# Performance work log

Measured on AMD Instinct MI355X. Metric: run time of the kernel, lower is better.

Reference implementation:

```python
import jax, jax.numpy as jnp
import numpy as np
from jax import lax

B, SEQ, CIN = 8, 4096, 7
DM, NL, PL = 512, 4, 16
NP = SEQ // PL            # 256 patches
NS, DC, EXP = 16, 4, 2
DI = EXP * DM             # 1024 inner dim
DTR = (DM + 15) // 16     # 32 dt_rank (mamba_ssm default ceil(d_model/16))
CD, PRED = 64, 96
EPS = 1e-5


def setup_inputs() -> dict:
    key = jax.random.key(0)
    ks = jax.random.split(key, 16)
    r = lambda k, s, sc=0.02: jax.random.normal(k, s, jnp.float32) * sc
    A_row = jnp.arange(1, NS + 1, dtype=jnp.float32)
    return {
        "x": jax.random.normal(ks[0], (B, SEQ, CIN), jnp.float32),
        "in_g": jnp.ones((CIN,), jnp.float32), "in_b": jnp.zeros((CIN,), jnp.float32),
        "pe_W": r(ks[1], (DM, CIN, PL), 0.1), "pe_b": jnp.zeros((DM,), jnp.float32),
        "ln_g": jnp.ones((NL, DM), jnp.float32), "ln_b": jnp.zeros((NL, DM), jnp.float32),
        "W_in": r(ks[2], (NL, 2 * DI, DM)),
        "conv_W": r(ks[3], (NL, DI, 1, DC), 0.2), "conv_b": jnp.zeros((NL, DI), jnp.float32),
        "W_x": r(ks[4], (NL, DTR + 2 * NS, DI)),
        "W_dt": r(ks[5], (NL, DI, DTR), 0.1),
        "b_dt": jnp.full((NL, DI), -4.6, jnp.float32),  # softplus^-1(~0.01)
        "A_log": jnp.log(jnp.tile(A_row, (NL, DI, 1))),
        "Dskip": jnp.ones((NL, DI), jnp.float32),
        "W_out": r(ks[6], (NL, DM, DI)),
        "fn_g": jnp.ones((DM,), jnp.float32), "fn_b": jnp.zeros((DM,), jnp.float32),
        "hW1": r(ks[7], (2 * CD, DM * NP)), "hb1": jnp.zeros((2 * CD,), jnp.float32),
        "hW2": r(ks[8], (PRED, 2 * CD)), "hb2": jnp.zeros((PRED,), jnp.float32),
    }


def layernorm(x, g, b):
    m = jnp.mean(x, axis=-1, keepdims=True)
    v = jnp.mean((x - m) ** 2, axis=-1, keepdims=True)
    return (x - m) * lax.rsqrt(v + EPS) * g + b


def silu(x):
    return x * jax.nn.sigmoid(x)


def selective_scan(dA, dBx, C):
    # dA, dBx: (B, L, DI, N);  C: (B, L, N)  ->  y: (B, L, DI)
    def step(h, t):
        dA_t, dbx_t, c_t = t
        h = dA_t * h + dbx_t                      # (B, DI, N)
        y = jnp.einsum('bdn,bn->bd', h, c_t)
        return h, y
    h0 = jnp.zeros((dA.shape[0], DI, NS), dA.dtype)
    _, ys = lax.scan(step, h0, (dA.transpose(1, 0, 2, 3), dBx.transpose(1, 0, 2, 3), C.transpose(1, 0, 2)))
    return ys.transpose(1, 0, 2)


def mamba_block(u, W_in, cW, cb, W_x, W_dt, b_dt, A_log, Dv, W_out):
    xz = jnp.einsum('bld,ed->ble', u, W_in)       # (B, L, 2*DI)
    xi, z = jnp.split(xz, 2, axis=-1)
    # causal depthwise conv over time
    xc = lax.conv_general_dilated(xi.transpose(0, 2, 1), cW, (1,), [(DC - 1, 0)],
                                  feature_group_count=DI,
                                  dimension_numbers=('NCH', 'OIH', 'NCH'))
    xc = silu(xc + cb[None, :, None]).transpose(0, 2, 1)  # (B, L, DI)
    dbl = jnp.einsum('bld,ed->ble', xc, W_x)      # (B, L, DTR + 2*NS)
    dt, Bm, Cm = dbl[..., :DTR], dbl[..., DTR:DTR + NS], dbl[..., DTR + NS:]
    delta = jax.nn.softplus(jnp.einsum('blr,dr->bld', dt, W_dt) + b_dt)  # (B, L, DI)
    A = -jnp.exp(A_log)                           # (DI, NS)
    dA = jnp.exp(delta[..., None] * A)            # (B, L, DI, NS)
    dBx = delta[..., None] * Bm[:, :, None, :] * xc[..., None]
    y = selective_scan(dA, dBx, Cm)
    y = (y + xc * Dv) * silu(z)
    return jnp.einsum('bld,od->blo', y, W_out)


def reference(x, in_g, in_b, pe_W, pe_b, ln_g, ln_b, W_in, conv_W, conv_b,
              W_x, W_dt, b_dt, A_log, Dskip, W_out, fn_g, fn_b, hW1, hb1, hW2, hb2):
    h = layernorm(x, in_g, in_b)
    # patch embed: stride==kernel Conv1d == per-patch matmul
    p = h.reshape(B, NP, PL, CIN)
    h = jnp.einsum('bnpc,dcp->bnd', p, pe_W) + pe_b   # (B, NP, DM)
    for i in range(NL):
        res = h
        h = layernorm(h, ln_g[i], ln_b[i])
        h = mamba_block(h, W_in[i], conv_W[i], conv_b[i], W_x[i], W_dt[i],
                        b_dt[i], A_log[i], Dskip[i], W_out[i])
        h = h + res                                   # dropout is identity at eval
    h = layernorm(h, fn_g, fn_b)
    h = h.reshape(B, -1)                              # (B, DM*NP)
    h = jax.nn.gelu(h @ hW1.T + hb1, approximate=False)
    return h @ hW2.T + hb2                            # (B, PRED)
```

## Files before the change

kernel.cpp:

```cpp
#include <hip/hip_runtime.h>
#include <hip/hip_bf16.h>
#include <math.h>

#define B_    8
#define SEQ_  4096
#define CIN_  7
#define DM_   512
#define NL_   4
#define PL_   16
#define NP_   256
#define NS_   16
#define DC_   4
#define DI_   1024
#define DTR_  32
#define CD_   64
#define PRED_ 96
#define TOK_  (B_*NP_)
#define EPS_  1e-5f
#define CL_   16
#define NCH_  (NP_/CL_)

typedef unsigned short u16;
typedef __attribute__((ext_vector_type(8))) short short8;
typedef __attribute__((ext_vector_type(4))) float floatx4;

__device__ __forceinline__ float silu_f(float x){ return x / (1.f + __expf(-x)); }
__device__ __forceinline__ float softplus_f(float x){ return x > 20.f ? x : log1pf(__expf(x)); }
__device__ __forceinline__ u16 f2bf(float f){
  union { __hip_bfloat16 h; u16 u; } cv; cv.h = __float2bfloat16(f); return cv.u;
}
#define GLDS16(g, l) __builtin_amdgcn_global_load_lds( \
    (const __attribute__((address_space(1))) void*)(g), \
    (__attribute__((address_space(3))) void*)(l), 16, 0, 0)

__global__ void ln7_kernel(const float* __restrict__ x, const float* __restrict__ g,
                           const float* __restrict__ b, u16* __restrict__ xpb){
  int i = blockIdx.x*256 + threadIdx.x;
  if (i >= B_*SEQ_) return;
  float v[CIN_]; float m = 0.f;
  #pragma unroll
  for (int c=0;c<CIN_;c++){ v[c]=x[i*CIN_+c]; m+=v[c]; }
  m *= (1.f/CIN_);
  float var = 0.f;
  #pragma unroll
  for (int c=0;c<CIN_;c++){ float d=v[c]-m; var+=d*d; }
  var *= (1.f/CIN_);
  float r = rsqrtf(var + EPS_);
  int bn = i >> 4, p = i & 15;
  u16* row = xpb + (size_t)bn*128;
  #pragma unroll
  for (int c=0;c<CIN_;c++) row[c*16+p] = f2bf((v[c]-m)*r*g[c]+b[c]);
  row[112+p] = 0;
}

__global__ __launch_bounds__(256) void ln512_kernel(const float* __restrict__ in,
    const float* __restrict__ g, const float* __restrict__ b,
    float* __restrict__ out, u16* __restrict__ outb){
  int tid = threadIdx.x;
  int wv = tid>>6, lane = tid&63;
  int t = blockIdx.x*4 + wv;
  const float4* row = (const float4*)(in + (size_t)t*DM_);
  float4 v0 = row[lane], v1 = row[64+lane];
  float s = v0.x+v0.y+v0.z+v0.w + v1.x+v1.y+v1.z+v1.w;
  #pragma unroll
  for (int o=1;o<64;o<<=1) s += __shfl_xor(s,o);
  float m = s*(1.f/DM_);
  float d0x=v0.x-m,d0y=v0.y-m,d0z=v0.z-m,d0w=v0.w-m;
  float d1x=v1.x-m,d1y=v1.y-m,d1z=v1.z-m,d1w=v1.w-m;
  float q = d0x*d0x+d0y*d0y+d0z*d0z+d0w*d0w + d1x*d1x+d1y*d1y+d1z*d1z+d1w*d1w;
  #pragma unroll
  for (int o=1;o<64;o<<=1) q += __shfl_xor(q,o);
  float r = rsqrtf(q*(1.f/DM_) + EPS_);
  float4 g0 = ((const float4*)g)[lane], g1 = ((const float4*)g)[64+lane];
  float4 b0 = ((const float4*)b)[lane], b1 = ((const float4*)b)[64+lane];
  float4 o0 = { d0x*r*g0.x+b0.x, d0y*r*g0.y+b0.y, d0z*r*g0.z+b0.z, d0w*r*g0.w+b0.w };
  float4 o1 = { d1x*r*g1.x+b1.x, d1y*r*g1.y+b1.y, d1z*r*g1.z+b1.z, d1w*r*g1.w+b1.w };
  ((float4*)(out + (size_t)t*DM_))[lane]    = o0;
  ((float4*)(out + (size_t)t*DM_))[64+lane] = o1;
  ushort4 p0 = { f2bf(o0.x), f2bf(o0.y), f2bf(o0.z), f2bf(o0.w) };
  ushort4 p1 = { f2bf(o1.x), f2bf(o1.y), f2bf(o1.z), f2bf(o1.w) };
  ((ushort4*)(outb + (size_t)t*DM_))[lane]    = p0;
  ((ushort4*)(outb + (size_t)t*DM_))[64+lane] = p1;
}

template<int BM, int BN, bool ACC, bool BIAS>
__global__ __launch_bounds__(256) void gemm_bf16(const u16* __restrict__ A,
    const u16* __restrict__ Bw, float* __restrict__ C, const float* __restrict__ bias,
    int K, int lda, int ldb, int ldc){
  constexpr int MI = BM/32, NI = BN/32;
  __shared__ __align__(16) u16 As[BM*64];
  __shared__ __align__(16) u16 Bs[BN*64];
  int tid = threadIdx.x;
  int wave = __builtin_amdgcn_readfirstlane(tid>>6);
  int lane = tid&63;
  int wm = wave>>1, wn = wave&1;
  int quad = lane>>4, l16 = lane&15;
  int bm = blockIdx.y*BM, bn = blockIdx.x*BN;
  int r8 = lane>>3, sseg = lane&7;
  int gseg = sseg ^ r8;
  floatx4 acc[MI][NI] = {};
  for (int k0 = 0; k0 < K; k0 += 64){
    #pragma unroll
    for (int r = 0; r < BM/32; r++){
      int rowb = (r*4 + wave)*8;
      const u16* gp = A + (size_t)(bm + rowb + r8)*lda + k0 + gseg*8;
      GLDS16(gp, &As[rowb*64]);
    }
    #pragma unroll
    for (int r = 0; r < BN/32; r++){
      int rowb = (r*4 + wave)*8;
      const u16* gp = Bw + (size_t)(bn + rowb + r8)*ldb + k0 + gseg*8;
      GLDS16(gp, &Bs[rowb*64]);
    }
    __syncthreads();
    #pragma unroll
    for (int kh = 0; kh < 2; kh++){
      short8 af[MI], bfr[NI];
      #pragma unroll
      for (int i = 0; i < MI; i++){
        int row = wm*(BM/2)+i*16+l16;
        af[i] = *(short8*)&As[row*64 + (((kh*4+quad)^(row&7))*8)];
      }
      #pragma unroll
      for (int j = 0; j < NI; j++){
        int row = wn*(BN/2)+j*16+l16;
        bfr[j] = *(short8*)&Bs[row*64 + (((kh*4+quad)^(row&7))*8)];
      }
      #pragma unroll
      for (int i = 0; i < MI; i++)
        #pragma unroll
        for (int j = 0; j < NI; j++)
          acc[i][j] = __builtin_amdgcn_mfma_f32_16x16x32_bf16(af[i], bfr[j], acc[i][j], 0, 0, 0);
    }
    __syncthreads();
  }
  #pragma unroll
  for (int i = 0; i < MI; i++){
    #pragma unroll
    for (int j = 0; j < NI; j++){
      #pragma unroll
      for (int r = 0; r < 4; r++){
        int m  = bm + wm*(BM/2) + i*16 + quad*4 + r;
        int nn = bn + wn*(BN/2) + j*16 + l16;
        float v = acc[i][j][r];
        if (ACC) C[(size_t)m*ldc+nn] += v;
        else     C[(size_t)m*ldc+nn]  = BIAS ? v + bias[nn] : v;
      }
    }
  }
}

__global__ __launch_bounds__(256) void dblpart_kernel(const u16* __restrict__ A,
    const u16* __restrict__ Bw, float* __restrict__ part){
  __shared__ __align__(16) u16 As[64*64];
  __shared__ __align__(16) u16 Bs[64*64];
  int tid = threadIdx.x;
  int wave = __builtin_amdgcn_readfirstlane(tid>>6);
  int lane = tid&63;
  int wm = wave>>1, wn = wave&1;
  int quad = lane>>4, l16 = lane&15;
  int bm = blockIdx.x*64;
  int kc = blockIdx.y;
  int r8 = lane>>3, sseg = lane&7;
  int gseg = sseg ^ r8;
  floatx4 acc[2][2] = {};
  for (int k0 = kc*256; k0 < kc*256 + 256; k0 += 64){
    #pragma unroll
    for (int r = 0; r < 2; r++){
      int rowb = (r*4 + wave)*8;
      GLDS16(A  + (size_t)(bm + rowb + r8)*DI_ + k0 + gseg*8, &As[rowb*64]);
      GLDS16(Bw + (size_t)(     rowb + r8)*DI_ + k0 + gseg*8, &Bs[rowb*64]);
    }
    __syncthreads();
    #pragma unroll
    for (int kh = 0; kh < 2; kh++){
      short8 af[2], bfr[2];
      #pragma unroll
      for (int i = 0; i < 2; i++){
        int row = wm*32+i*16+l16;
        af[i] = *(short8*)&As[row*64 + (((kh*4+quad)^(row&7))*8)];
      }
      #pragma unroll
      for (int j = 0; j < 2; j++){
        int row = wn*32+j*16+l16;
        bfr[j] = *(short8*)&Bs[row*64 + (((kh*4+quad)^(row&7))*8)];
      }
      #pragma unroll
      for (int i = 0; i < 2; i++)
        #pragma unroll
        for (int j = 0; j < 2; j++)
          acc[i][j] = __builtin_amdgcn_mfma_f32_16x16x32_bf16(af[i], bfr[j], acc[i][j], 0, 0, 0);
    }
    __syncthreads();
  }
  float* dst = part + (size_t)kc*TOK_*64;
  #pragma unroll
  for (int i = 0; i < 2; i++)
    #pragma unroll
    for (int j = 0; j < 2; j++)
      #pragma unroll
      for (int r = 0; r < 4; r++){
        int m  = bm + wm*32 + i*16 + quad*4 + r;
        int nn = wn*32 + j*16 + l16;
        dst[(size_t)m*64+nn] = acc[i][j][r];
      }
}

__global__ __launch_bounds__(256) void dblsum_kernel(const float* __restrict__ part,
    float* __restrict__ dbl){
  int idx = blockIdx.x*256 + threadIdx.x;
  float4 a = ((const float4*)part)[idx];
  float4 b = ((const float4*)(part + (size_t)TOK_*64))[idx];
  float4 c = ((const float4*)(part + (size_t)2*TOK_*64))[idx];
  float4 d = ((const float4*)(part + (size_t)3*TOK_*64))[idx];
  float4 o = { a.x+b.x+c.x+d.x, a.y+b.y+c.y+d.y, a.z+b.z+c.z+d.z, a.w+b.w+c.w+d.w };
  ((float4*)dbl)[idx] = o;
}

__global__ void conv_silu_kernel(const float* __restrict__ xz, const float* __restrict__ cW,
                                 const float* __restrict__ cb, float* __restrict__ xc,
                                 u16* __restrict__ xcb){
  int idx = blockIdx.x*256 + threadIdx.x;
  if (idx >= TOK_*DI_/4) return;
  int c4 = idx & (DI_/4 - 1); int t = idx >> 8;
  int l = t & (NP_-1);
  int c = c4*4;
  float4 acc = *(const float4*)&cb[c];
  float wa[4], wb[4], wc[4], wd[4];
  *(float4*)wa = *(const float4*)&cW[(c+0)*DC_];
  *(float4*)wb = *(const float4*)&cW[(c+1)*DC_];
  *(float4*)wc = *(const float4*)&cW[(c+2)*DC_];
  *(float4*)wd = *(const float4*)&cW[(c+3)*DC_];
  const float* base = xz + (size_t)t*(2*DI_) + c;
  #pragma unroll
  for (int k = 0; k < DC_; k++){
    if (l - 3 + k >= 0){
      float4 xv = *(const float4*)(base + (k-3)*(2*DI_));
      acc.x += xv.x*wa[k];
      acc.y += xv.y*wb[k];
      acc.z += xv.z*wc[k];
      acc.w += xv.w*wd[k];
    }
  }
  acc.x = silu_f(acc.x); acc.y = silu_f(acc.y);
  acc.z = silu_f(acc.z); acc.w = silu_f(acc.w);
  *(float4*)&xc[(size_t)t*DI_ + c] = acc;
  ushort4 pb = { f2bf(acc.x), f2bf(acc.y), f2bf(acc.z), f2bf(acc.w) };
  *(ushort4*)&xcb[(size_t)t*DI_ + c] = pb;
}

__global__ __launch_bounds__(256) void delta_kernel(const float* __restrict__ dbl,
    const float* __restrict__ wdtT, const float* __restrict__ bdt, float* __restrict__ delta){
  __shared__ float sdt[16][DTR_];
  int tid = threadIdx.x;
  int t0 = blockIdx.y*16;
  int d = blockIdx.x*256 + tid;
  for (int i = tid; i < 16*DTR_; i += 256){
    int t = i >> 5, r = i & 31;
    sdt[t][r] = dbl[(size_t)(t0 + t)*64 + r];
  }
  float wv[DTR_];
  #pragma unroll
  for (int r = 0; r < DTR_; r++) wv[r] = wdtT[(size_t)r*DI_ + d];
  float bb = bdt[d];
  __syncthreads();
  #pragma unroll 4
  for (int t = 0; t < 16; t++){
    float acc = bb;
    #pragma unroll
    for (int r = 0; r < DTR_; r++) acc += sdt[t][r]*wv[r];
    delta[(size_t)(t0 + t)*DI_ + d] = softplus_f(acc);
  }
}

__global__ __launch_bounds__(256) void scan_part_kernel(const float* __restrict__ delta,
    const float* __restrict__ xc, const float* __restrict__ dbl,
    const float* __restrict__ Alog, float* __restrict__ hend, float* __restrict__ aprod){
  __shared__ float sBC[CL_][32];
  int tid = threadIdx.x;
  int d = blockIdx.x*256 + tid;
  int bych = blockIdx.y;
  int b = bych >> 4, ch = bych & (NCH_-1);
  int base = b*NP_ + ch*CL_;
  for (int i = tid; i < CL_*32; i += 256){
    int t = i >> 5, c = i & 31;
    sBC[t][c] = dbl[(size_t)(base+t)*64 + 32 + c];
  }
  float A[NS_], h[NS_], pr[NS_];
  #pragma unroll
  for (int k = 0; k < NS_; k++){
    A[k] = -__expf(Alog[(size_t)d*NS_ + k]);
    h[k] = 0.f; pr[k] = 1.f;
  }
  __syncthreads();
  #pragma unroll
  for (int t = 0; t < CL_; t++){
    int row = base + t;
    float de = delta[(size_t)row*DI_ + d];
    float xv = xc[(size_t)row*DI_ + d];
    float cde = de*xv;
    #pragma unroll
    for (int k = 0; k < NS_; k++){
      float a = __expf(de*A[k]);
      h[k] = a*h[k] + cde*sBC[t][k];
      pr[k] *= a;
    }
  }
  size_t o = ((size_t)bych*DI_ + d)*NS_;
  #pragma unroll
  for (int k = 0; k < NS_; k++){ hend[o+k] = h[k]; aprod[o+k] = pr[k]; }
}

__global__ __launch_bounds__(256) void scan_fix_kernel(const float* __restrict__ aprod,
    float* __restrict__ hend){
  int id = blockIdx.x*256 + threadIdx.x;
  int nd = id & (DI_*NS_ - 1);
  int b  = id >> 14;
  float h = 0.f;
  #pragma unroll
  for (int ch = 0; ch < NCH_; ch++){
    size_t idx = (size_t)(b*NCH_ + ch)*(DI_*NS_) + nd;
    float ap = aprod[idx];
    float he = hend[idx];
    hend[idx] = h;
    h = ap*h + he;
  }
}

__global__ __launch_bounds__(256) void scan_final_kernel(const float* __restrict__ delta,
    const float* __restrict__ xc, const float* __restrict__ dbl,
    const float* __restrict__ xz, const float* __restrict__ Dv,
    const float* __restrict__ Alog, const float* __restrict__ hin,
    u16* __restrict__ yb){
  __shared__ float sBC[CL_][32];
  int tid = threadIdx.x;
  int d = blockIdx.x*256 + tid;
  int bych = blockIdx.y;
  int b = bych >> 4, ch = bych & (NCH_-1);
  int base = b*NP_ + ch*CL_;
  for (int i = tid; i < CL_*32; i += 256){
    int t = i >> 5, c = i & 31;
    sBC[t][c] = dbl[(size_t)(base+t)*64 + 32 + c];
  }
  float A[NS_], h[NS_];
  size_t o = ((size_t)bych*DI_ + d)*NS_;
  #pragma unroll
  for (int k = 0; k < NS_; k++){
    A[k] = -__expf(Alog[(size_t)d*NS_ + k]);
    h[k] = hin[o + k];
  }
  float Dvd = Dv[d];
  __syncthreads();
  #pragma unroll
  for (int t = 0; t < CL_; t++){
    int row = base + t;
    float de = delta[(size_t)row*DI_ + d];
    float xv = xc[(size_t)row*DI_ + d];
    float zz = xz[(size_t)row*(2*DI_) + DI_ + d];
    float cde = de*xv;
    float p = 0.f;
    #pragma unroll
    for (int k = 0; k < NS_; k++){
      float a = __expf(de*A[k]);
      h[k] = a*h[k] + cde*sBC[t][k];
      p += h[k]*sBC[t][16+k];
    }
    yb[(size_t)row*DI_ + d] = f2bf((p + xv*Dvd) * silu_f(zz));
  }
}

__global__ __launch_bounds__(256) void head1_kernel(const float* __restrict__ u,
    const float* __restrict__ hW1, float* __restrict__ partial){
  const int KTOT = DM_*NP_;
  int nb = blockIdx.x;
  int kc = blockIdx.y;
  int tid = threadIdx.x;
  int lane = tid & 63, wv = tid >> 6;
  int n = nb*4 + wv;
  const float* wrow = hW1 + (size_t)n*KTOT;
  float acc[8] = {};
  int kb = kc*1024 + lane*4;
  #pragma unroll
  for (int it = 0; it < 4; it++){
    int k = kb + it*256;
    float4 w4 = *(const float4*)&wrow[k];
    #pragma unroll
    for (int m = 0; m < 8; m++){
      float4 u4 = *(const float4*)&u[(size_t)m*KTOT + k];
      acc[m] += u4.x*w4.x + u4.y*w4.y + u4.z*w4.z + u4.w*w4.w;
    }
  }
  #pragma unroll
  for (int m = 0; m < 8; m++){
    float v = acc[m];
    v += __shfl_xor(v,1); v += __shfl_xor(v,2); v += __shfl_xor(v,4);
    v += __shfl_xor(v,8); v += __shfl_xor(v,16); v += __shfl_xor(v,32);
    acc[m] = v;
  }
  if (lane == 0){
    float* dst = partial + ((size_t)kc*128 + n)*8;
    #pragma unroll
    for (int m = 0; m < 8; m++) dst[m] = acc[m];
  }
}

__global__ void head_combine_kernel(const float* __restrict__ partial,
    const float* __restrict__ hb1, float* __restrict__ t1){
  int idx = blockIdx.x*256 + threadIdx.x;
  if (idx >= 128*8) return;
  int n = idx >> 3, m = idx & 7;
  float s = hb1[n];
  for (int kc = 0; kc < 128; kc++) s += partial[((size_t)kc*128 + n)*8 + m];
  float ge = 0.5f*s*(1.f + erff(s*0.70710678118f));
  t1[m*128 + n] = ge;
}

__global__ void head2_kernel(const float* __restrict__ t1, const float* __restrict__ hW2,
                             const float* __restrict__ hb2, float* __restrict__ out){
  int idx = blockIdx.x*128 + threadIdx.x;
  if (idx >= B_*PRED_) return;
  int m = idx / PRED_, q = idx % PRED_;
  float s = hb2[q];
  #pragma unroll 16
  for (int k = 0; k < 2*CD_; k++) s += t1[m*128 + k]*hW2[q*128 + k];
  out[idx] = s;
}

__global__ __launch_bounds__(256) void prep_kernel(const float* __restrict__ W_dt,
    const float* __restrict__ W_x, const float* __restrict__ W_in,
    const float* __restrict__ W_out, const float* __restrict__ peW,
    float* __restrict__ wdtT, u16* __restrict__ wxB,
    u16* __restrict__ WinB, u16* __restrict__ WoutB, u16* __restrict__ peWb){
  int idx = blockIdx.x*256 + threadIdx.x;
  {
    float4 v = ((const float4*)W_in)[idx];
    ushort4 o = { f2bf(v.x), f2bf(v.y), f2bf(v.z), f2bf(v.w) };
    ((ushort4*)WinB)[idx] = o;
  }
  if (idx < 524288){
    float4 v = ((const float4*)W_out)[idx];
    ushort4 o = { f2bf(v.x), f2bf(v.y), f2bf(v.z), f2bf(v.w) };
    ((ushort4*)WoutB)[idx] = o;
  }
  if (idx < NL_*64*DI_/4){
    float4 v = ((const float4*)W_x)[idx];
    ushort4 o = { f2bf(v.x), f2bf(v.y), f2bf(v.z), f2bf(v.w) };
    ((ushort4*)wxB)[idx] = o;
  }
  if (idx < NL_*DTR_*DI_){
    int l = idx / (DTR_*DI_); int rem = idx % (DTR_*DI_);
    int r = rem / DI_; int d = rem % DI_;
    wdtT[idx] = W_dt[((size_t)l*DI_ + d)*DTR_ + r];
  }
  if (idx < 512*128){
    int d = idx >> 7, kk = idx & 127;
    peWb[idx] = (kk < 112) ? f2bf(peW[d*112 + kk]) : (u16)0;
  }
}

extern "C" void kernel_launch(void* const* d_in, const int* in_sizes, int n_in,
                              void* d_out, int out_size, void* d_ws, size_t ws_size,
                              hipStream_t stream) {
  const float* x      = (const float*)d_in[0];
  const float* in_g   = (const float*)d_in[1];
  const float* in_b   = (const float*)d_in[2];
  const float* pe_W   = (const float*)d_in[3];
  const float* pe_b   = (const float*)d_in[4];
  const float* ln_g   = (const float*)d_in[5];
  const float* ln_b   = (const float*)d_in[6];
  const float* W_in   = (const float*)d_in[7];
  const float* conv_W = (const float*)d_in[8];
  const float* conv_b = (const float*)d_in[9];
  const float* W_x    = (const float*)d_in[10];
  const float* W_dt   = (const float*)d_in[11];
  const float* b_dt   = (const float*)d_in[12];
  const float* A_log  = (const float*)d_in[13];
  const float* Dskip  = (const float*)d_in[14];
  const float* W_out  = (const float*)d_in[15];
  const float* fn_g   = (const float*)d_in[16];
  const float* fn_b   = (const float*)d_in[17];
  const float* hW1    = (const float*)d_in[18];
  const float* hb1    = (const float*)d_in[19];
  const float* hW2    = (const float*)d_in[20];
  const float* hb2    = (const float*)d_in[21];

  float* ws    = (float*)d_ws;
  float* h     = ws;
  float* un    = h     + 1048576;
  float* xz    = un    + 1048576;
  float* xc    = xz    + 4194304;
  float* dblb  = xc    + 2097152;
  float* delta = dblb  + 131072;
  float* y     = delta + 2097152;
  float* wdtT  = y     + 2097152;
  u16*   wxB   = (u16*)(wdtT + 131072);
  float* bf_rgn= wdtT + 131072 + 131072;
  u16*   unb   = (u16*)bf_rgn;
  u16*   yb    = (u16*)(bf_rgn + 524288);
  u16*   WinB  = (u16*)(bf_rgn + 524288 + 1048576);
  u16*   WoutB = (u16*)(bf_rgn + 524288 + 1048576 + 2097152);
  u16*   peWb  = (u16*)(bf_rgn + 524288 + 1048576 + 2097152 + 1048576);
  float* aprod = bf_rgn + 524288 + 1048576 + 2097152 + 1048576 + 32768;
  float* hend  = y;
  u16*   xcb   = (u16*)y;
  u16*   xpb   = (u16*)y;
  float* dblpart = aprod;
  float* partial = xz;
  float* t1      = xz + 262144;

  prep_kernel<<<4096, 256, 0, stream>>>(W_dt, W_x, W_in, W_out, pe_W,
                                        wdtT, wxB, WinB, WoutB, peWb);
  ln7_kernel<<<(B_*SEQ_+255)/256, 256, 0, stream>>>(x, in_g, in_b, xpb);
  gemm_bf16<64,128,false,true><<<dim3(DM_/128, TOK_/64), 256, 0, stream>>>(
      xpb, peWb, h, pe_b, 128, 128, 128, DM_);

  for (int l = 0; l < NL_; l++){
    ln512_kernel<<<TOK_/4, 256, 0, stream>>>(h, ln_g + l*DM_, ln_b + l*DM_, un, unb);
    gemm_bf16<64,128,false,false><<<dim3(2*DI_/128, TOK_/64), 256, 0, stream>>>(
        unb, WinB + (size_t)l*2*DI_*DM_, xz, nullptr, DM_, DM_, DM_, 2*DI_);
    conv_silu_kernel<<<(TOK_*DI_/4)/256, 256, 0, stream>>>(
        xz, conv_W + (size_t)l*DI_*DC_, conv_b + (size_t)l*DI_, xc, xcb);
    dblpart_kernel<<<dim3(TOK_/64, 4), 256, 0, stream>>>(
        xcb, wxB + (size_t)l*64*DI_, dblpart);
    dblsum_kernel<<<(TOK_*64/4)/256, 256, 0, stream>>>(dblpart, dblb);
    delta_kernel<<<dim3(DI_/256, TOK_/16), 256, 0, stream>>>(
        dblb, wdtT + (size_t)l*DTR_*DI_, b_dt + (size_t)l*DI_, delta);
    scan_part_kernel<<<dim3(DI_/256, B_*NCH_), 256, 0, stream>>>(
        delta, xc, dblb, A_log + (size_t)l*DI_*NS_, hend, aprod);
    scan_fix_kernel<<<(B_*DI_*NS_)/256, 256, 0, stream>>>(aprod, hend);
    scan_final_kernel<<<dim3(DI_/256, B_*NCH_), 256, 0, stream>>>(
        delta, xc, dblb, xz, Dskip + (size_t)l*DI_, A_log + (size_t)l*DI_*NS_, hend, yb);
    gemm_bf16<64,64,true,false><<<dim3(DM_/64, TOK_/64), 256, 0, stream>>>(
        yb, WoutB + (size_t)l*DM_*DI_, h, nullptr, DI_, DI_, DI_, DM_);
  }

  ln512_kernel<<<TOK_/4, 256, 0, stream>>>(h, fn_g, fn_b, un, unb);
  head1_kernel<<<dim3(32, 128), 256, 0, stream>>>(un, hW1, partial);
  head_combine_kernel<<<4, 256, 0, stream>>>(partial, hb1, t1);
  head2_kernel<<<6, 128, 0, stream>>>(t1, hW2, hb2, (float*)d_out);
}
```

Measured before the change: 576.5 us.

## Drop fp32 intermediates, fuse dbl reduction into delta, MFMA head GEMM

Removes the fp32 copies of the layernorm output and the conv/silu output, so scan kernels read the bf16 xc instead. The separate dblsum kernel is folded into delta_kernel, which sums the four partials on the fly and writes the B/C part once. The head's first GEMM is rewritten to convert hW1 to bf16 on the fly and use MFMA over 512 K-chunks with a two-stage reduction. This cuts memory traffic and launches but adds bf16 rounding of xc in the scan and of hW1/activations in the head, plus redundant partial sums across delta blocks.

```diff
diff --git a/kernel.cpp b/kernel.cpp
--- a/kernel.cpp
+++ b/kernel.cpp
@@ -16,6 +16,7 @@
 #define CD_   64
 #define PRED_ 96
 #define TOK_  (B_*NP_)
+#define KTOT_ (DM_*NP_)
 #define EPS_  1e-5f
 #define CL_   16
 #define NCH_  (NP_/CL_)
@@ -28,6 +29,9 @@
 __device__ __forceinline__ float softplus_f(float x){ return x > 20.f ? x : log1pf(__expf(x)); }
 __device__ __forceinline__ u16 f2bf(float f){
   union { __hip_bfloat16 h; u16 u; } cv; cv.h = __float2bfloat16(f); return cv.u;
+}
+__device__ __forceinline__ float bf2f(u16 u){
+  union { unsigned int i; float f; } cv; cv.i = ((unsigned int)u) << 16; return cv.f;
 }
 #define GLDS16(g, l) __builtin_amdgcn_global_load_lds( \
     (const __attribute__((address_space(1))) void*)(g), \
@@ -54,8 +58,7 @@
 }
 
 __global__ __launch_bounds__(256) void ln512_kernel(const float* __restrict__ in,
-    const float* __restrict__ g, const float* __restrict__ b,
-    float* __restrict__ out, u16* __restrict__ outb){
+    const float* __restrict__ g, const float* __restrict__ b, u16* __restrict__ outb){
   int tid = threadIdx.x;
   int wv = tid>>6, lane = tid&63;
   int t = blockIdx.x*4 + wv;
@@ -75,8 +78,6 @@
   float4 b0 = ((const float4*)b)[lane], b1 = ((const float4*)b)[64+lane];
   float4 o0 = { d0x*r*g0.x+b0.x, d0y*r*g0.y+b0.y, d0z*r*g0.z+b0.z, d0w*r*g0.w+b0.w };
   float4 o1 = { d1x*r*g1.x+b1.x, d1y*r*g1.y+b1.y, d1z*r*g1.z+b1.z, d1w*r*g1.w+b1.w };
-  ((float4*)(out + (size_t)t*DM_))[lane]    = o0;
-  ((float4*)(out + (size_t)t*DM_))[64+lane] = o1;
   ushort4 p0 = { f2bf(o0.x), f2bf(o0.y), f2bf(o0.z), f2bf(o0.w) };
   ushort4 p1 = { f2bf(o1.x), f2bf(o1.y), f2bf(o1.z), f2bf(o1.w) };
   ((ushort4*)(outb + (size_t)t*DM_))[lane]    = p0;
@@ -206,20 +207,8 @@
       }
 }
 
-__global__ __launch_bounds__(256) void dblsum_kernel(const float* __restrict__ part,
-    float* __restrict__ dbl){
-  int idx = blockIdx.x*256 + threadIdx.x;
-  float4 a = ((const float4*)part)[idx];
-  float4 b = ((const float4*)(part + (size_t)TOK_*64))[idx];
-  float4 c = ((const float4*)(part + (size_t)2*TOK_*64))[idx];
-  float4 d = ((const float4*)(part + (size_t)3*TOK_*64))[idx];
-  float4 o = { a.x+b.x+c.x+d.x, a.y+b.y+c.y+d.y, a.z+b.z+c.z+d.z, a.w+b.w+c.w+d.w };
-  ((float4*)dbl)[idx] = o;
-}
-
 __global__ void conv_silu_kernel(const float* __restrict__ xz, const float* __restrict__ cW,
-                                 const float* __restrict__ cb, float* __restrict__ xc,
-                                 u16* __restrict__ xcb){
+                                 const float* __restrict__ cb, u16* __restrict__ xcb){
   int idx = blockIdx.x*256 + threadIdx.x;
   if (idx >= TOK_*DI_/4) return;
   int c4 = idx & (DI_/4 - 1); int t = idx >> 8;
@@ -242,22 +231,32 @@
       acc.w += xv.w*wd[k];
     }
   }
-  acc.x = silu_f(acc.x); acc.y = silu_f(acc.y);
-  acc.z = silu_f(acc.z); acc.w = silu_f(acc.w);
-  *(float4*)&xc[(size_t)t*DI_ + c] = acc;
-  ushort4 pb = { f2bf(acc.x), f2bf(acc.y), f2bf(acc.z), f2bf(acc.w) };
+  ushort4 pb = { f2bf(silu_f(acc.x)), f2bf(silu_f(acc.y)),
+                 f2bf(silu_f(acc.z)), f2bf(silu_f(acc.w)) };
   *(ushort4*)&xcb[(size_t)t*DI_ + c] = pb;
 }
 
-__global__ __launch_bounds__(256) void delta_kernel(const float* __restrict__ dbl,
-    const float* __restrict__ wdtT, const float* __restrict__ bdt, float* __restrict__ delta){
+__global__ __launch_bounds__(256) void delta_kernel(const float* __restrict__ part,
+    const float* __restrict__ wdtT, const float* __restrict__ bdt,
+    float* __restrict__ dbl, float* __restrict__ delta){
   __shared__ float sdt[16][DTR_];
   int tid = threadIdx.x;
   int t0 = blockIdx.y*16;
-  int d = blockIdx.x*256 + tid;
-  for (int i = tid; i < 16*DTR_; i += 256){
+  int dx = blockIdx.x;
+  int d = dx*256 + tid;
+  for (int i = tid; i < 16*32; i += 256){
     int t = i >> 5, r = i & 31;
-    sdt[t][r] = dbl[(size_t)(t0 + t)*64 + r];
+    size_t o = (size_t)(t0 + t)*64 + r;
+    sdt[t][r] = part[o] + part[(size_t)TOK_*64 + o]
+              + part[(size_t)2*TOK_*64 + o] + part[(size_t)3*TOK_*64 + o];
+  }
+  if (dx == 0){
+    for (int i = tid; i < 16*32; i += 256){
+      int t = i >> 5, c = i & 31;
+      size_t o = (size_t)(t0 + t)*64 + 32 + c;
+      dbl[o] = part[o] + part[(size_t)TOK_*64 + o]
+             + part[(size_t)2*TOK_*64 + o] + part[(size_t)3*TOK_*64 + o];
+    }
   }
   float wv[DTR_];
   #pragma unroll
@@ -274,7 +273,7 @@
 }
 
 __global__ __launch_bounds__(256) void scan_part_kernel(const float* __restrict__ delta,
-    const float* __restrict__ xc, const float* __restrict__ dbl,
+    const u16* __restrict__ xcb, const float* __restrict__ dbl,
     const float* __restrict__ Alog, float* __restrict__ hend, float* __restrict__ aprod){
   __shared__ float sBC[CL_][32];
   int tid = threadIdx.x;
@@ -297,7 +296,7 @@
   for (int t = 0; t < CL_; t++){
     int row = base + t;
     float de = delta[(size_t)row*DI_ + d];
-    float xv = xc[(size_t)row*DI_ + d];
+    float xv = bf2f(xcb[(size_t)row*DI_ + d]);
     float cde = de*xv;
     #pragma unroll
     for (int k = 0; k < NS_; k++){
@@ -328,7 +327,7 @@
 }
 
 __global__ __launch_bounds__(256) void scan_final_kernel(const float* __restrict__ delta,
-    const float* __restrict__ xc, const float* __restrict__ dbl,
+    const u16* __restrict__ xcb, const float* __restrict__ dbl,
     const float* __restrict__ xz, const float* __restrict__ Dv,
     const float* __restrict__ Alog, const float* __restrict__ hin,
     u16* __restrict__ yb){
@@ -355,7 +354,7 @@
   for (int t = 0; t < CL_; t++){
     int row = base + t;
     float de = delta[(size_t)row*DI_ + d];
-    float xv = xc[(size_t)row*DI_ + d];
+    float xv = bf2f(xcb[(size_t)row*DI_ + d]);
     float zz = xz[(size_t)row*(2*DI_) + DI_ + d];
     float cde = de*xv;
     float p = 0.f;
@@ -369,48 +368,76 @@
   }
 }
 
-__global__ __launch_bounds__(256) void head1_kernel(const float* __restrict__ u,
-    const float* __restrict__ hW1, float* __restrict__ partial){
-  const int KTOT = DM_*NP_;
-  int nb = blockIdx.x;
-  int kc = blockIdx.y;
-  int tid = threadIdx.x;
-  int lane = tid & 63, wv = tid >> 6;
-  int n = nb*4 + wv;
-  const float* wrow = hW1 + (size_t)n*KTOT;
-  float acc[8] = {};
-  int kb = kc*1024 + lane*4;
-  #pragma unroll
-  for (int it = 0; it < 4; it++){
-    int k = kb + it*256;
-    float4 w4 = *(const float4*)&wrow[k];
-    #pragma unroll
-    for (int m = 0; m < 8; m++){
-      float4 u4 = *(const float4*)&u[(size_t)m*KTOT + k];
-      acc[m] += u4.x*w4.x + u4.y*w4.y + u4.z*w4.z + u4.w*w4.w;
-    }
-  }
-  #pragma unroll
-  for (int m = 0; m < 8; m++){
-    float v = acc[m];
-    v += __shfl_xor(v,1); v += __shfl_xor(v,2); v += __shfl_xor(v,4);
-    v += __shfl_xor(v,8); v += __shfl_xor(v,16); v += __shfl_xor(v,32);
-    acc[m] = v;
-  }
-  if (lane == 0){
-    float* dst = partial + ((size_t)kc*128 + n)*8;
-    #pragma unroll
-    for (int m = 0; m < 8; m++) dst[m] = acc[m];
-  }
-}
-
-__global__ void head_combine_kernel(const float* __restrict__ partial,
+__global__ __launch_bounds__(256) void head1_kernel(const float* __restrict__ hW1,
+    const u16* __restrict__ ub, float* __restrict__ partial){
+  __shared__ __align__(16) u16 As[128*64];
+  __shared__ __align__(16) u16 Bs[16*64];
+  int tid = threadIdx.x;
+  int wave = __builtin_amdgcn_readfirstlane(tid>>6);
+  int lane = tid & 63, quad = lane>>4, l16 = lane&15;
+  int kc = blockIdx.x;
+  int arow = tid & 127, apair = tid >> 7;
+  floatx4 acc[2] = {};
+  for (int sc = 0; sc < 4; sc++){
+    int k0 = kc*256 + sc*64;
+    const float* ap = hW1 + (size_t)arow*KTOT_ + k0 + apair*32;
+    #pragma unroll
+    for (int s = 0; s < 4; s++){
+      float4 f0 = *(const float4*)(ap + s*8);
+      float4 f1 = *(const float4*)(ap + s*8 + 4);
+      union { u16 h[8]; int4 v; } pk;
+      pk.h[0]=f2bf(f0.x); pk.h[1]=f2bf(f0.y); pk.h[2]=f2bf(f0.z); pk.h[3]=f2bf(f0.w);
+      pk.h[4]=f2bf(f1.x); pk.h[5]=f2bf(f1.y); pk.h[6]=f2bf(f1.z); pk.h[7]=f2bf(f1.w);
+      int seg = apair*4 + s;
+      *(int4*)&As[arow*64 + ((seg^(arow&7))*8)] = pk.v;
+    }
+    if (tid < 128){
+      int brow = tid >> 3, bseg = tid & 7;
+      int4 bv = {0,0,0,0};
+      if (brow < 8) bv = *(const int4*)&ub[(size_t)brow*KTOT_ + k0 + bseg*8];
+      *(int4*)&Bs[brow*64 + ((bseg^(brow&7))*8)] = bv;
+    }
+    __syncthreads();
+    #pragma unroll
+    for (int kh = 0; kh < 2; kh++){
+      short8 bf = *(short8*)&Bs[l16*64 + (((kh*4+quad)^(l16&7))*8)];
+      #pragma unroll
+      for (int i = 0; i < 2; i++){
+        int row = wave*32 + i*16 + l16;
+        short8 af = *(short8*)&As[row*64 + (((kh*4+quad)^(row&7))*8)];
+        acc[i] = __builtin_amdgcn_mfma_f32_16x16x32_bf16(af, bf, acc[i], 0, 0, 0);
+      }
+    }
+    __syncthreads();
+  }
+  if (l16 < 8){
+    #pragma unroll
+    for (int i = 0; i < 2; i++)
+      #pragma unroll
+      for (int r = 0; r < 4; r++){
+        int n = wave*32 + i*16 + quad*4 + r;
+        partial[(size_t)kc*1024 + n*8 + l16] = acc[i][r];
+      }
+  }
+}
+
+__global__ void head_comb1_kernel(const float* __restrict__ partial, float* __restrict__ pp2){
+  int out = blockIdx.x*256 + threadIdx.x;
+  int g = blockIdx.y;
+  const float* p = partial + (size_t)g*64*1024 + out;
+  float s = 0.f;
+  #pragma unroll 8
+  for (int j = 0; j < 64; j++) s += p[(size_t)j*1024];
+  pp2[g*1024 + out] = s;
+}
+
+__global__ void head_comb2_kernel(const float* __restrict__ pp2,
     const float* __restrict__ hb1, float* __restrict__ t1){
-  int idx = blockIdx.x*256 + threadIdx.x;
-  if (idx >= 128*8) return;
-  int n = idx >> 3, m = idx & 7;
+  int out = blockIdx.x*256 + threadIdx.x;
+  int n = out >> 3, m = out & 7;
   float s = hb1[n];
-  for (int kc = 0; kc < 128; kc++) s += partial[((size_t)kc*128 + n)*8 + m];
+  #pragma unroll
+  for (int g = 0; g < 8; g++) s += pp2[g*1024 + out];
   float ge = 0.5f*s*(1.f + erff(s*0.70710678118f));
   t1[m*128 + n] = ge;
 }
@@ -502,11 +529,12 @@
   u16*   peWb  = (u16*)(bf_rgn + 524288 + 1048576 + 2097152 + 1048576);
   float* aprod = bf_rgn + 524288 + 1048576 + 2097152 + 1048576 + 32768;
   float* hend  = y;
-  u16*   xcb   = (u16*)y;
+  u16*   xcb   = (u16*)xc;
   u16*   xpb   = (u16*)y;
   float* dblpart = aprod;
   float* partial = xz;
-  float* t1      = xz + 262144;
+  float* pp2     = xz + 524288;
+  float* t1      = xz + 532480;
 
   prep_kernel<<<4096, 256, 0, stream>>>(W_dt, W_x, W_in, W_out, pe_W,
                                         wdtT, wxB, WinB, WoutB, peWb);
@@ -515,27 +543,27 @@
       xpb, peWb, h, pe_b, 128, 128, 128, DM_);
 
   for (int l = 0; l < NL_; l++){
-    ln512_kernel<<<TOK_/4, 256, 0, stream>>>(h, ln_g + l*DM_, ln_b + l*DM_, un, unb);
+    ln512_kernel<<<TOK_/4, 256, 0, stream>>>(h, ln_g + l*DM_, ln_b + l*DM_, unb);
     gemm_bf16<64,128,false,false><<<dim3(2*DI_/128, TOK_/64), 256, 0, stream>>>(
         unb, WinB + (size_t)l*2*DI_*DM_, xz, nullptr, DM_, DM_, DM_, 2*DI_);
     conv_silu_kernel<<<(TOK_*DI_/4)/256, 256, 0, stream>>>(
-        xz, conv_W + (size_t)l*DI_*DC_, conv_b + (size_t)l*DI_, xc, xcb);
+        xz, conv_W + (size_t)l*DI_*DC_, conv_b + (size_t)l*DI_, xcb);
     dblpart_kernel<<<dim3(TOK_/64, 4), 256, 0, stream>>>(
         xcb, wxB + (size_t)l*64*DI_, dblpart);
-    dblsum_kernel<<<(TOK_*64/4)/256, 256, 0, stream>>>(dblpart, dblb);
     delta_kernel<<<dim3(DI_/256, TOK_/16), 256, 0, stream>>>(
-        dblb, wdtT + (size_t)l*DTR_*DI_, b_dt + (size_t)l*DI_, delta);
+        dblpart, wdtT + (size_t)l*DTR_*DI_, b_dt + (size_t)l*DI_, dblb, delta);
     scan_part_kernel<<<dim3(DI_/256, B_*NCH_), 256, 0, stream>>>(
-        delta, xc, dblb, A_log + (size_t)l*DI_*NS_, hend, aprod);
+        delta, xcb, dblb, A_log + (size_t)l*DI_*NS_, hend, aprod);
     scan_fix_kernel<<<(B_*DI_*NS_)/256, 256, 0, stream>>>(aprod, hend);
     scan_final_kernel<<<dim3(DI_/256, B_*NCH_), 256, 0, stream>>>(
-        delta, xc, dblb, xz, Dskip + (size_t)l*DI_, A_log + (size_t)l*DI_*NS_, hend, yb);
+        delta, xcb, dblb, xz, Dskip + (size_t)l*DI_, A_log + (size_t)l*DI_*NS_, hend, yb);
     gemm_bf16<64,64,true,false><<<dim3(DM_/64, TOK_/64), 256, 0, stream>>>(
         yb, WoutB + (size_t)l*DM_*DI_, h, nullptr, DI_, DI_, DI_, DM_);
   }
 
-  ln512_kernel<<<TOK_/4, 256, 0, stream>>>(h, fn_g, fn_b, un, unb);
-  head1_kernel<<<dim3(32, 128), 256, 0, stream>>>(un, hW1, partial);
-  head_combine_kernel<<<4, 256, 0, stream>>>(partial, hb1, t1);
+  ln512_kernel<<<TOK_/4, 256, 0, stream>>>(h, fn_g, fn_b, unb);
+  head1_kernel<<<512, 256, 0, stream>>>(hW1, unb, partial);
+  head_comb1_kernel<<<dim3(4, 8), 256, 0, stream>>>(partial, pp2);
+  head_comb2_kernel<<<4, 256, 0, stream>>>(pp2, hb1, t1);
   head2_kernel<<<6, 128, 0, stream>>>(t1, hW2, hb2, (float*)d_out);
 }
```

New measurement: 553.1 us. -4.1%, faster.
